# Kernel tuning notes

Measured on AMD Instinct MI355X. Metric: run time of the kernel, lower is better.

The kernel has to match this reference:

```python
import jax, jax.numpy as jnp
import numpy as np

B, L, D = 4, 4096, 1024
K_LEN = 128  # decay kernel taps


def setup_inputs() -> dict:
    key = jax.random.key(0)
    k1, k2, k3 = jax.random.split(key, 3)
    x = jax.random.normal(k1, (B, L, D), dtype=jnp.float32)
    W_qkv = jax.random.normal(k2, (3 * D, D), dtype=jnp.float32) * 0.02
    W_out = jax.random.normal(k3, (D, D), dtype=jnp.float32) * 0.02
    # matches torch init: exp(-linspace(0, 10, 128))
    decay_kernel = jnp.exp(-jnp.linspace(0.0, 10.0, K_LEN)).astype(jnp.float32)
    return {"x": x, "W_qkv": W_qkv, "W_out": W_out, "decay_kernel": decay_kernel}


def reference(x, W_qkv, W_out, decay_kernel):
    # qkv projection (bias=False): [B,L,D] @ [D,3D] -> split into q,k,v
    qkv = jnp.einsum('bld,ed->ble', x, W_qkv)
    q, k, v = jnp.split(qkv, 3, axis=-1)
    src = k * v  # [B,L,D]
    K = decay_kernel.shape[0]
    N = x.shape[1] + K - 1  # full linear-conv length
    src_f = jnp.fft.rfft(src, n=N, axis=1)                 # [B,N//2+1,D] complex
    kern_f = jnp.fft.rfft(decay_kernel, n=N)[None, :, None]  # same kernel per channel
    res = jnp.fft.irfft(src_f * kern_f, n=N, axis=1)[:, :x.shape[1], :]  # causal slice
    out = q * res  # q-gating
    # dropout is identity in eval mode
    return jnp.einsum('bld,ed->ble', out, W_out)
```

## Files before the change

### kernel.cpp

```cpp
#include <hip/hip_runtime.h>

#define BDIM 4
#define LDIM 4096
#define DDIM 1024
#define KTAPS 128
#define LCHUNK 64

typedef __attribute__((ext_vector_type(8))) _Float16 f16x8;
typedef __attribute__((ext_vector_type(16))) float f32x16;

__device__ __forceinline__ float f16_to_f(ushort h) {
    return (float)__builtin_bit_cast(_Float16, h);
}
__device__ __forceinline__ ushort f_to_f16(float f) {
    return __builtin_bit_cast(ushort, (_Float16)f);
}
__device__ __forceinline__ uint pack2(float lo, float hi) {
    return (uint)f_to_f16(lo) | ((uint)f_to_f16(hi) << 16);
}

__device__ __forceinline__ void load_lds16(const ushort* g, ushort* l) {
    __builtin_amdgcn_global_load_lds(
        (const __attribute__((address_space(1))) void*)g,
        (__attribute__((address_space(3))) void*)l, 16, 0, 0);
}

#define NX8 (BDIM * LDIM * DDIM / 8)
#define NQ8 (3 * DDIM * DDIM / 8)
#define NO8 (DDIM * DDIM / 8)
__global__ __launch_bounds__(256) void to_f16_all(const float* __restrict__ x,
                                                  const float* __restrict__ wq,
                                                  const float* __restrict__ wo,
                                                  ushort* __restrict__ xh,
                                                  ushort* __restrict__ wqh,
                                                  ushort* __restrict__ woh) {
    const int ntot = NX8 + NQ8 + NO8;
    for (int i = blockIdx.x * 256 + threadIdx.x; i < ntot; i += gridDim.x * 256) {
        const float* src;
        ushort* dst;
        int j = i;
        if (j < NX8) {
            src = x; dst = xh;
        } else if (j < NX8 + NQ8) {
            j -= NX8; src = wq; dst = wqh;
        } else {
            j -= NX8 + NQ8; src = wo; dst = woh;
        }
        const float4 v0 = *(const float4*)&src[(size_t)j * 8];
        const float4 v1 = *(const float4*)&src[(size_t)j * 8 + 4];
        uint4 h;
        h.x = pack2(v0.x, v0.y);
        h.y = pack2(v0.z, v0.w);
        h.z = pack2(v1.x, v1.y);
        h.w = pack2(v1.z, v1.w);
        *(uint4*)&dst[(size_t)j * 8] = h;
    }
}

template <int OBF>
__global__ __launch_bounds__(256) void gemm_f16(const ushort* __restrict__ A,
                                                const ushort* __restrict__ B,
                                                void* __restrict__ Cp, int ldc, int Kc) {
    __shared__ ushort As[128 * 64];
    __shared__ ushort Bs[128 * 64];

    const int tid = threadIdx.x;

    const int gx = gridDim.x;
    const int nwg = gx * gridDim.y;
    const int orig = blockIdx.y * gx + blockIdx.x;
    const int q8 = nwg >> 3;
    const int tile = (orig & 7) * q8 + (orig >> 3);
    const int m0 = (tile / gx) * 128;
    const int n0 = (tile % gx) * 128;

    const int srow = tid >> 3;
    const int osrc = (tid & 7) ^ (srow & 7);

    const ushort* srcA = A + (size_t)(m0 + srow) * Kc + osrc * 8;
    const ushort* srcB = B + (size_t)(n0 + srow) * Kc + osrc * 8;

    const int lane = tid & 63;
    const int w = tid >> 6;
    const int wr = w >> 1, wc = w & 1;
    const int l31 = lane & 31;
    const int hi = lane >> 5;
    const int swz = l31 & 7;
    const int arow = wr * 64 + l31;
    const int brow = wc * 64 + l31;

    f32x16 acc[2][2] = {};

    for (int kc = 0; kc < Kc; kc += 64) {
        __syncthreads();
#pragma unroll
        for (int s = 0; s < 4; ++s) {
            const size_t so = (size_t)(s * 32) * Kc + kc;
            load_lds16(srcA + so, &As[s * 2048 + tid * 8]);
            load_lds16(srcB + so, &Bs[s * 2048 + tid * 8]);
        }
        __syncthreads();

#pragma unroll
        for (int ks = 0; ks < 4; ++ks) {
            const int oph = ((2 * ks + hi) ^ swz) * 8;
            f16x8 a0 = *(const f16x8*)&As[arow * 64 + oph];
            f16x8 a1 = *(const f16x8*)&As[(arow + 32) * 64 + oph];
            f16x8 b0 = *(const f16x8*)&Bs[brow * 64 + oph];
            f16x8 b1 = *(const f16x8*)&Bs[(brow + 32) * 64 + oph];
            acc[0][0] = __builtin_amdgcn_mfma_f32_32x32x16_f16(a0, b0, acc[0][0], 0, 0, 0);
            acc[0][1] = __builtin_amdgcn_mfma_f32_32x32x16_f16(a0, b1, acc[0][1], 0, 0, 0);
            acc[1][0] = __builtin_amdgcn_mfma_f32_32x32x16_f16(a1, b0, acc[1][0], 0, 0, 0);
            acc[1][1] = __builtin_amdgcn_mfma_f32_32x32x16_f16(a1, b1, acc[1][1], 0, 0, 0);
        }
    }

#pragma unroll
    for (int rb = 0; rb < 2; ++rb)
#pragma unroll
        for (int cb = 0; cb < 2; ++cb) {
            const int colb = n0 + wc * 64 + cb * 32 + l31;
            const int rowb = m0 + wr * 64 + rb * 32 + 4 * hi;
#pragma unroll
            for (int q = 0; q < 16; ++q) {
                const int row = rowb + (q & 3) + 8 * (q >> 2);
                if (OBF) {
                    ((ushort*)Cp)[(size_t)row * ldc + colb] = f_to_f16(acc[rb][cb][q]);
                } else {
                    ((float*)Cp)[(size_t)row * ldc + colb] = acc[rb][cb][q];
                }
            }
        }
}

__device__ __forceinline__ float2 up2(uint u) {
    return make_float2(f16_to_f((ushort)(u & 0xffff)), f16_to_f((ushort)(u >> 16)));
}

__global__ __launch_bounds__(256) void conv_gate_f16(const ushort* __restrict__ qkvh,
                                                     const float* __restrict__ decay,
                                                     ushort* __restrict__ gh) {
    __shared__ float sdec[KTAPS];
    if (threadIdx.x < KTAPS) sdec[threadIdx.x] = decay[threadIdx.x];
    __syncthreads();

    const int dp = blockIdx.y * 256 + threadIdx.x;
    const int b = blockIdx.z;
    const int l0 = blockIdx.x * LCHUNK;

    const float r = sdec[1];
    const int rsu = 3 * DDIM / 2;
    const int gsu = DDIM / 2;

    const uint* basep = (const uint*)(qkvh + (size_t)b * LDIM * 3 * DDIM);
    const uint* qc = basep + dp;
    const uint* kc = basep + DDIM / 2 + dp;
    const uint* vc = basep + DDIM + dp;
    uint* g0 = (uint*)(gh + (size_t)b * LDIM * DDIM) + dp;

    float res0 = 0.f, res1 = 0.f;
    int lstart;

    if (l0 == 0) {
        lstart = 0;
    } else {
        const int tmax = (l0 < KTAPS - 1) ? l0 : (KTAPS - 1);
#pragma unroll 4
        for (int t = 0; t <= tmax; ++t) {
            const size_t off = (size_t)(l0 - t) * rsu;
            const float2 kk = up2(kc[off]), vv = up2(vc[off]);
            res0 += sdec[t] * kk.x * vv.x;
            res1 += sdec[t] * kk.y * vv.y;
        }
        const float2 qq = up2(qc[(size_t)l0 * rsu]);
        g0[(size_t)l0 * gsu] = pack2(qq.x * res0, qq.y * res1);
        lstart = l0 + 1;
    }

    for (int l = lstart; l < l0 + LCHUNK; ++l) {
        const size_t off = (size_t)l * rsu;
        const float2 kk = up2(kc[off]), vv = up2(vc[off]);
        res0 = r * res0 + kk.x * vv.x;
        res1 = r * res1 + kk.y * vv.y;
        const float2 qq = up2(qc[off]);
        g0[(size_t)l * gsu] = pack2(qq.x * res0, qq.y * res1);
    }
}

extern "C" void kernel_launch(void* const* d_in, const int* in_sizes, int n_in,
                              void* d_out, int out_size, void* d_ws, size_t ws_size,
                              hipStream_t stream) {
    const float* x = (const float*)d_in[0];
    const float* Wqkv = (const float*)d_in[1];
    const float* Wout = (const float*)d_in[2];
    const float* decay = (const float*)d_in[3];

    const int M = BDIM * LDIM;
    const size_t MB = 1024 * 1024;

    ushort* qkvh = (ushort*)d_ws;
    ushort* gh = (ushort*)((char*)d_ws + 96 * MB);
    ushort* xh = (ushort*)((char*)d_ws + 128 * MB);
    ushort* wqkvh = (ushort*)((char*)d_ws + 160 * MB);
    ushort* wouth = (ushort*)((char*)d_ws + 166 * MB);

    to_f16_all<<<2048, 256, 0, stream>>>(x, Wqkv, Wout, xh, wqkvh, wouth);

    dim3 g1(3 * DDIM / 128, M / 128);
    gemm_f16<1><<<g1, 256, 0, stream>>>(xh, wqkvh, qkvh, 3 * DDIM, DDIM);

    dim3 g2(LDIM / LCHUNK, 2, BDIM);
    conv_gate_f16<<<g2, 256, 0, stream>>>(qkvh, decay, gh);

    dim3 g3(DDIM / 128, M / 128);
    gemm_f16<0><<<g3, 256, 0, stream>>>(gh, wouth, d_out, DDIM, DDIM);
}
```

Before: 237.5 us.

## Fuse k*v product into QKV GEMM epilogue via interleaved weight rows

Interleaves the k and v rows of the QKV weight during the fp16 conversion so adjacent output columns hold matching k and v channels. The first GEMM's epilogue multiplies each pair with a lane shuffle and writes only q and k*v, cutting the intermediate from 3D to 2D columns. The conv/gate kernel then reads one source stream instead of two. This lowers global write and read traffic at the cost of extra shuffles in the epilogue and half the lanes idling on the k*v stores.

```diff
diff --git a/kernel.cpp b/kernel.cpp
--- a/kernel.cpp
+++ b/kernel.cpp
@@ -35,16 +35,25 @@
                                                   ushort* __restrict__ wqh,
                                                   ushort* __restrict__ woh) {
     const int ntot = NX8 + NQ8 + NO8;
+    const int OPR = DDIM / 8;
     for (int i = blockIdx.x * 256 + threadIdx.x; i < ntot; i += gridDim.x * 256) {
         const float* src;
         ushort* dst;
         int j = i;
+        int jd;
         if (j < NX8) {
-            src = x; dst = xh;
+            src = x; dst = xh; jd = j;
         } else if (j < NX8 + NQ8) {
             j -= NX8; src = wq; dst = wqh;
+            const int row = j >> 7;
+            const int c8 = j & 127;
+            int dr;
+            if (row < 1024) dr = row;
+            else if (row < 2048) dr = 1024 + 2 * (row - 1024);
+            else dr = 1024 + 2 * (row - 2048) + 1;
+            jd = dr * OPR + c8;
         } else {
-            j -= NX8 + NQ8; src = wo; dst = woh;
+            j -= NX8 + NQ8; src = wo; dst = woh; jd = j;
         }
         const float4 v0 = *(const float4*)&src[(size_t)j * 8];
         const float4 v1 = *(const float4*)&src[(size_t)j * 8 + 4];
@@ -53,14 +62,13 @@
         h.y = pack2(v0.z, v0.w);
         h.z = pack2(v1.x, v1.y);
         h.w = pack2(v1.z, v1.w);
-        *(uint4*)&dst[(size_t)j * 8] = h;
-    }
-}
-
-template <int OBF>
-__global__ __launch_bounds__(256) void gemm_f16(const ushort* __restrict__ A,
+        *(uint4*)&dst[(size_t)jd * 8] = h;
+    }
+}
+
+__global__ __launch_bounds__(256) void gemm1_qs(const ushort* __restrict__ A,
                                                 const ushort* __restrict__ B,
-                                                void* __restrict__ Cp, int ldc, int Kc) {
+                                                ushort* __restrict__ qs, int Kc) {
     __shared__ ushort As[128 * 64];
     __shared__ ushort Bs[128 * 64];
 
@@ -115,6 +123,99 @@
         }
     }
 
+    if (n0 < 1024) {
+#pragma unroll
+        for (int rb = 0; rb < 2; ++rb)
+#pragma unroll
+            for (int cb = 0; cb < 2; ++cb) {
+                const int colb = n0 + wc * 64 + cb * 32 + l31;
+                const int rowb = m0 + wr * 64 + rb * 32 + 4 * hi;
+#pragma unroll
+                for (int q = 0; q < 16; ++q) {
+                    const int row = rowb + (q & 3) + 8 * (q >> 2);
+                    qs[(size_t)row * 2048 + colb] = f_to_f16(acc[rb][cb][q]);
+                }
+            }
+    } else {
+        const bool isK = (l31 & 1) == 0;
+#pragma unroll
+        for (int rb = 0; rb < 2; ++rb)
+#pragma unroll
+            for (int cb = 0; cb < 2; ++cb) {
+                const int gcol = (n0 - 1024) + wc * 64 + cb * 32 + l31;
+                const int scol = 1024 + (gcol >> 1);
+                const int rowb = m0 + wr * 64 + rb * 32 + 4 * hi;
+#pragma unroll
+                for (int q = 0; q < 16; ++q) {
+                    const float mine = acc[rb][cb][q];
+                    const float partner = __shfl_xor(mine, 1);
+                    if (isK) {
+                        const int row = rowb + (q & 3) + 8 * (q >> 2);
+                        qs[(size_t)row * 2048 + scol] = f_to_f16(mine * partner);
+                    }
+                }
+            }
+    }
+}
+
+template <int OBF>
+__global__ __launch_bounds__(256) void gemm_f16(const ushort* __restrict__ A,
+                                                const ushort* __restrict__ B,
+                                                void* __restrict__ Cp, int ldc, int Kc) {
+    __shared__ ushort As[128 * 64];
+    __shared__ ushort Bs[128 * 64];
+
+    const int tid = threadIdx.x;
+
+    const int gx = gridDim.x;
+    const int nwg = gx * gridDim.y;
+    const int orig = blockIdx.y * gx + blockIdx.x;
+    const int q8 = nwg >> 3;
+    const int tile = (orig & 7) * q8 + (orig >> 3);
+    const int m0 = (tile / gx) * 128;
+    const int n0 = (tile % gx) * 128;
+
+    const int srow = tid >> 3;
+    const int osrc = (tid & 7) ^ (srow & 7);
+
+    const ushort* srcA = A + (size_t)(m0 + srow) * Kc + osrc * 8;
+    const ushort* srcB = B + (size_t)(n0 + srow) * Kc + osrc * 8;
+
+    const int lane = tid & 63;
+    const int w = tid >> 6;
+    const int wr = w >> 1, wc = w & 1;
+    const int l31 = lane & 31;
+    const int hi = lane >> 5;
+    const int swz = l31 & 7;
+    const int arow = wr * 64 + l31;
+    const int brow = wc * 64 + l31;
+
+    f32x16 acc[2][2] = {};
+
+    for (int kc = 0; kc < Kc; kc += 64) {
+        __syncthreads();
+#pragma unroll
+        for (int s = 0; s < 4; ++s) {
+            const size_t so = (size_t)(s * 32) * Kc + kc;
+            load_lds16(srcA + so, &As[s * 2048 + tid * 8]);
+            load_lds16(srcB + so, &Bs[s * 2048 + tid * 8]);
+        }
+        __syncthreads();
+
+#pragma unroll
+        for (int ks = 0; ks < 4; ++ks) {
+            const int oph = ((2 * ks + hi) ^ swz) * 8;
+            f16x8 a0 = *(const f16x8*)&As[arow * 64 + oph];
+            f16x8 a1 = *(const f16x8*)&As[(arow + 32) * 64 + oph];
+            f16x8 b0 = *(const f16x8*)&Bs[brow * 64 + oph];
+            f16x8 b1 = *(const f16x8*)&Bs[(brow + 32) * 64 + oph];
+            acc[0][0] = __builtin_amdgcn_mfma_f32_32x32x16_f16(a0, b0, acc[0][0], 0, 0, 0);
+            acc[0][1] = __builtin_amdgcn_mfma_f32_32x32x16_f16(a0, b1, acc[0][1], 0, 0, 0);
+            acc[1][0] = __builtin_amdgcn_mfma_f32_32x32x16_f16(a1, b0, acc[1][0], 0, 0, 0);
+            acc[1][1] = __builtin_amdgcn_mfma_f32_32x32x16_f16(a1, b1, acc[1][1], 0, 0, 0);
+        }
+    }
+
 #pragma unroll
     for (int rb = 0; rb < 2; ++rb)
 #pragma unroll
@@ -137,7 +238,7 @@
     return make_float2(f16_to_f((ushort)(u & 0xffff)), f16_to_f((ushort)(u >> 16)));
 }
 
-__global__ __launch_bounds__(256) void conv_gate_f16(const ushort* __restrict__ qkvh,
+__global__ __launch_bounds__(256) void conv_gate_f16(const ushort* __restrict__ qsb,
                                                      const float* __restrict__ decay,
                                                      ushort* __restrict__ gh) {
     __shared__ float sdec[KTAPS];
@@ -149,13 +250,12 @@
     const int l0 = blockIdx.x * LCHUNK;
 
     const float r = sdec[1];
-    const int rsu = 3 * DDIM / 2;
+    const int rsu = 1024;
     const int gsu = DDIM / 2;
 
-    const uint* basep = (const uint*)(qkvh + (size_t)b * LDIM * 3 * DDIM);
+    const uint* basep = (const uint*)(qsb + (size_t)b * LDIM * 2048);
     const uint* qc = basep + dp;
-    const uint* kc = basep + DDIM / 2 + dp;
-    const uint* vc = basep + DDIM + dp;
+    const uint* sc = basep + 512 + dp;
     uint* g0 = (uint*)(gh + (size_t)b * LDIM * DDIM) + dp;
 
     float res0 = 0.f, res1 = 0.f;
@@ -167,10 +267,9 @@
         const int tmax = (l0 < KTAPS - 1) ? l0 : (KTAPS - 1);
 #pragma unroll 4
         for (int t = 0; t <= tmax; ++t) {
-            const size_t off = (size_t)(l0 - t) * rsu;
-            const float2 kk = up2(kc[off]), vv = up2(vc[off]);
-            res0 += sdec[t] * kk.x * vv.x;
-            res1 += sdec[t] * kk.y * vv.y;
+            const float2 ss = up2(sc[(size_t)(l0 - t) * rsu]);
+            res0 += sdec[t] * ss.x;
+            res1 += sdec[t] * ss.y;
         }
         const float2 qq = up2(qc[(size_t)l0 * rsu]);
         g0[(size_t)l0 * gsu] = pack2(qq.x * res0, qq.y * res1);
@@ -178,11 +277,10 @@
     }
 
     for (int l = lstart; l < l0 + LCHUNK; ++l) {
-        const size_t off = (size_t)l * rsu;
-        const float2 kk = up2(kc[off]), vv = up2(vc[off]);
-        res0 = r * res0 + kk.x * vv.x;
-        res1 = r * res1 + kk.y * vv.y;
-        const float2 qq = up2(qc[off]);
+        const float2 ss = up2(sc[(size_t)l * rsu]);
+        res0 = r * res0 + ss.x;
+        res1 = r * res1 + ss.y;
+        const float2 qq = up2(qc[(size_t)l * rsu]);
         g0[(size_t)l * gsu] = pack2(qq.x * res0, qq.y * res1);
     }
 }
@@ -198,19 +296,19 @@
     const int M = BDIM * LDIM;
     const size_t MB = 1024 * 1024;
 
-    ushort* qkvh = (ushort*)d_ws;
-    ushort* gh = (ushort*)((char*)d_ws + 96 * MB);
-    ushort* xh = (ushort*)((char*)d_ws + 128 * MB);
-    ushort* wqkvh = (ushort*)((char*)d_ws + 160 * MB);
-    ushort* wouth = (ushort*)((char*)d_ws + 166 * MB);
+    ushort* qs = (ushort*)d_ws;
+    ushort* gh = (ushort*)((char*)d_ws + 64 * MB);
+    ushort* xh = (ushort*)((char*)d_ws + 96 * MB);
+    ushort* wqkvh = (ushort*)((char*)d_ws + 128 * MB);
+    ushort* wouth = (ushort*)((char*)d_ws + 134 * MB);
 
     to_f16_all<<<2048, 256, 0, stream>>>(x, Wqkv, Wout, xh, wqkvh, wouth);
 
     dim3 g1(3 * DDIM / 128, M / 128);
-    gemm_f16<1><<<g1, 256, 0, stream>>>(xh, wqkvh, qkvh, 3 * DDIM, DDIM);
+    gemm1_qs<<<g1, 256, 0, stream>>>(xh, wqkvh, qs, DDIM);
 
     dim3 g2(LDIM / LCHUNK, 2, BDIM);
-    conv_gate_f16<<<g2, 256, 0, stream>>>(qkvh, decay, gh);
+    conv_gate_f16<<<g2, 256, 0, stream>>>(qs, decay, gh);
 
     dim3 g3(DDIM / 128, M / 128);
     gemm_f16<0><<<g3, 256, 0, stream>>>(gh, wouth, d_out, DDIM, DDIM);
```

Result: no change. 235.7 us (median of 2 runs) (-0.7%).
